# Performance work log

Hardware: AMD Instinct MI355X
Metric: run time of the kernel (lower is better)

## Reference

```python
import jax, jax.numpy as jnp
import numpy as np

# Static configuration (mirrors init_kwargs / forward defaults)
KERNEL = 128          # WW
INDEX_BACK = 32768    # number of highest-frequency bins discarded
PADDING = 0           # padding_count (padding=None in forward)

def next_power2(x):
    return int(2 ** np.ceil(np.log2(x)))

def setup_inputs() -> dict:
    key = jax.random.key(0)
    k1, k2, k3 = jax.random.split(key, 3)
    N, C, W = 32, 8, 65536
    F = 16
    x = jax.random.normal(k1, (N, C, W), dtype=jnp.float32)
    weight = jax.random.normal(k2, (F, C, KERNEL), dtype=jnp.float32) * 0.1
    bias = jax.random.normal(k3, (F,), dtype=jnp.float32)
    return {"x": x, "weight": weight, "bias": bias}

def reference(x, weight, bias):
    # x: [N, C, W], weight: [F, C, WW], bias: [F]
    N, C, W = x.shape
    F, _, WW = weight.shape
    pad = PADDING
    out_W = W - WW + 1 + 2 * pad
    # fft size sized to also hold the backward dout correlation, then next pow2
    init_fft_size_input = W + 2 * pad + 2 * (WW - 1)
    init_fft_size_dout = out_W + 2 * (WW - 1)
    init_fft_size = next_power2(max(init_fft_size_input, init_fft_size_dout))
    half = init_fft_size // 2 + 1

    # rfft with implicit zero-padding to init_fft_size (input left-padded by `pad`)
    x_p = jnp.pad(x, ((0, 0), (0, 0), (pad, 0)))
    xfft = jnp.fft.rfft(x_p, n=init_fft_size, axis=-1)      # [N, C, half]
    yfft = jnp.fft.rfft(weight, n=init_fft_size, axis=-1)   # [F, C, half]

    # spectral compression: drop the INDEX_BACK highest-frequency bins
    keep = half - INDEX_BACK
    xfft = xfft[..., :keep]
    yfft = yfft[..., :keep]

    # cross-correlation in frequency domain (torch conv == correlation),
    # summing over input channels C in the spectrum (linearity of irfft)
    outfft = jnp.einsum('nck,fck->nfk', xfft, jnp.conj(yfft))  # [N, F, keep]

    # zero-pad discarded high frequencies back and invert
    outfft = jnp.pad(outfft, ((0, 0), (0, 0), (0, half - keep)))
    out = jnp.fft.irfft(outfft, n=init_fft_size, axis=-1)[..., :out_W]  # [N, F, out_W]

    out = out + bias[None, :, None]
    return out
```

## Files before the change

kernel.cpp:

```cpp
#include <hip/hip_runtime.h>

namespace {

constexpr int NFFT  = 65536;
constexpr int OUTW  = 65409;
constexpr size_t Y2BYTES = (size_t)256 * 129 * 128 * 8;

typedef float2 cplx;

__device__ __forceinline__ cplx cmk(float x, float y){ return make_float2(x, y); }
__device__ __forceinline__ cplx cadd(cplx a, cplx b){ return cmk(a.x+b.x, a.y+b.y); }
__device__ __forceinline__ cplx csub(cplx a, cplx b){ return cmk(a.x-b.x, a.y-b.y); }
__device__ __forceinline__ cplx cmul(cplx a, cplx b){ return cmk(a.x*b.x - a.y*b.y, a.x*b.y + a.y*b.x); }
__device__ __forceinline__ cplx cmulj(cplx a, cplx b){
  return cmk(a.x*b.x + a.y*b.y, a.y*b.x - a.x*b.y); }

template<int DIR>
__device__ __forceinline__ void dft16(cplx v[16]) {
  const float C1 = 0.92387953251128674f;
  const float S1 = 0.38268343236508977f;
  const float C2 = 0.70710678118654752f;
  const float WR[16]  = {1.f, C1, C2, S1, 0.f, -S1, -C2, -C1, -1.f, -C1, -C2, -S1, 0.f, S1, C2, C1};
  const float WIF[16] = {0.f, -S1, -C2, -C1, -1.f, -C1, -C2, -S1, 0.f, S1, C2, C1, 1.f, C1, C2, S1};
  cplx s[16];
  #pragma unroll
  for (int n2 = 0; n2 < 4; ++n2) {
    cplx a = v[n2], b = v[n2+4], c = v[n2+8], d = v[n2+12];
    cplx ac = cadd(a,c), am = csub(a,c), bd = cadd(b,d), bm = csub(b,d);
    cplx x0 = cadd(ac, bd), x2 = csub(ac, bd), x1, x3;
    if (DIR == -1) { x1 = cmk(am.x + bm.y, am.y - bm.x); x3 = cmk(am.x - bm.y, am.y + bm.x); }
    else           { x1 = cmk(am.x - bm.y, am.y + bm.x); x3 = cmk(am.x + bm.y, am.y - bm.x); }
    s[0*4+n2] = x0;
    {
      int e1 = (n2*1) & 15, e2 = (n2*2) & 15, e3 = (n2*3) & 15;
      cplx w1 = cmk(WR[e1], (DIR==-1)? WIF[e1] : -WIF[e1]);
      cplx w2 = cmk(WR[e2], (DIR==-1)? WIF[e2] : -WIF[e2]);
      cplx w3 = cmk(WR[e3], (DIR==-1)? WIF[e3] : -WIF[e3]);
      s[1*4+n2] = cmul(x1, w1);
      s[2*4+n2] = cmul(x2, w2);
      s[3*4+n2] = cmul(x3, w3);
    }
  }
  #pragma unroll
  for (int t1 = 0; t1 < 4; ++t1) {
    cplx a = s[t1*4+0], b = s[t1*4+1], c = s[t1*4+2], d = s[t1*4+3];
    cplx ac = cadd(a,c), am = csub(a,c), bd = cadd(b,d), bm = csub(b,d);
    cplx x0 = cadd(ac,bd), x2 = csub(ac,bd), x1, x3;
    if (DIR == -1) { x1 = cmk(am.x + bm.y, am.y - bm.x); x3 = cmk(am.x - bm.y, am.y + bm.x); }
    else           { x1 = cmk(am.x - bm.y, am.y + bm.x); x3 = cmk(am.x + bm.y, am.y - bm.x); }
    v[t1+0] = x0; v[t1+4] = x1; v[t1+8] = x2; v[t1+12] = x3;
  }
}

template<int DIR>
__global__ __launch_bounds__(256)
void fft_pass_a(const cplx* __restrict__ in, long inStride, int inLen,
                cplx* __restrict__ T) {
  int blk = blockIdx.x;
  int seq = blk >> 4;
  int B0  = (blk & 15) << 4;
  int t = threadIdx.x;
  __shared__ cplx sm[4608];
  cplx (*tile)[260] = (cplx(*)[260])sm;
  cplx* tile2 = sm;
  {
    const cplx* src = in + (long)seq * inStride;
    int cb = t & 15, rg = t >> 4;
    #pragma unroll
    for (int i = 0; i < 16; ++i) {
      int a = i*16 + rg;
      int sIdx = a*256 + B0 + cb;
      cplx v = (sIdx < inLen) ? src[sIdx] : cmk(0.f, 0.f);
      tile[cb][a] = v;
    }
  }
  __syncthreads();
  int cc = t >> 4, j = t & 15;
  cplx x[16];
  #pragma unroll
  for (int a1 = 0; a1 < 16; ++a1) x[a1] = tile[cc][a1*16 + j];
  dft16<DIR>(x);
  {
    float sn, cs;
    __sincosf((float)DIR * 6.28318530717958648f * (float)j * (1.0f/256.0f), &sn, &cs);
    cplx r = cmk(cs, sn), cur = r;
    #pragma unroll
    for (int t1 = 1; t1 < 16; ++t1) { x[t1] = cmul(x[t1], cur); cur = cmul(cur, r); }
  }
  __syncthreads();
  #pragma unroll
  for (int t1 = 0; t1 < 16; ++t1) tile[cc][t1*16 + ((j + t1) & 15)] = x[t1];
  __syncthreads();
  #pragma unroll
  for (int a2 = 0; a2 < 16; ++a2) x[a2] = tile[cc][j*16 + ((a2 + j) & 15)];
  dft16<DIR>(x);
  int b = B0 + cc;
  __syncthreads();
  {
    float sn, cs;
    __sincosf((float)DIR * 6.28318530717958648f * (float)(b*j) * (1.0f/65536.0f), &sn, &cs);
    cplx cur = cmk(cs, sn);
    __sincosf((float)DIR * 6.28318530717958648f * (float)b * (1.0f/4096.0f), &sn, &cs);
    cplx stp = cmk(cs, sn);
    #pragma unroll
    for (int t2 = 0; t2 < 16; ++t2) {
      tile2[(j + 16*t2)*18 + cc] = cmul(x[t2], cur);
      cur = cmul(cur, stp);
    }
  }
  __syncthreads();
  {
    int rg = t >> 4, cb = t & 15;
    cplx* dst = T + (long)seq * NFFT + B0 + cb;
    #pragma unroll
    for (int i = 0; i < 16; ++i) {
      int k1 = i*16 + rg;
      dst[(long)k1 * 256] = tile2[k1*18 + cb];
    }
  }
}

template<int DIR, int MODE>
__global__ __launch_bounds__(256)
void fft_pass_b(const cplx* __restrict__ T, cplx* __restrict__ outZ,
                float* __restrict__ outR, const float* __restrict__ bias,
                int seqBase) {
  int blk = blockIdx.x;
  int seq = blk >> 4;
  int K0  = (blk & 15) << 4;
  int t = threadIdx.x;
  __shared__ cplx tile[16][260];
  {
    const cplx* src = T + (long)seq * NFFT;
    int ck = t & 15, rg = t >> 4;
    #pragma unroll
    for (int i = 0; i < 16; ++i) {
      int b = i*16 + rg;
      tile[ck][b] = src[b*256 + K0 + ck];
    }
  }
  __syncthreads();
  int cc = t >> 4, j = t & 15;
  cplx x[16];
  #pragma unroll
  for (int a1 = 0; a1 < 16; ++a1) x[a1] = tile[cc][a1*16 + j];
  dft16<DIR>(x);
  {
    float sn, cs;
    __sincosf((float)DIR * 6.28318530717958648f * (float)j * (1.0f/256.0f), &sn, &cs);
    cplx r = cmk(cs, sn), cur = r;
    #pragma unroll
    for (int t1 = 1; t1 < 16; ++t1) { x[t1] = cmul(x[t1], cur); cur = cmul(cur, r); }
  }
  __syncthreads();
  #pragma unroll
  for (int t1 = 0; t1 < 16; ++t1) tile[cc][t1*16 + ((j + t1) & 15)] = x[t1];
  __syncthreads();
  #pragma unroll
  for (int a2 = 0; a2 < 16; ++a2) x[a2] = tile[cc][j*16 + ((a2 + j) & 15)];
  dft16<DIR>(x);
  __syncthreads();
  #pragma unroll
  for (int t2 = 0; t2 < 16; ++t2) tile[cc][j + 16*t2] = x[t2];
  __syncthreads();
  int ck2 = t & 15, rg2 = t >> 4;
  if (MODE == 0) {
    cplx* dst = outZ + (long)seq * NFFT + K0 + ck2;
    #pragma unroll
    for (int i = 0; i < 16; ++i) {
      int k2 = i*16 + rg2;
      dst[256*k2] = tile[ck2][k2];
    }
  } else {
    const float sc = 1.0f / 65536.0f;
    int gseq = seqBase + seq;
    float bf = bias[gseq & 15];
    float* dst = outR + (long)gseq * OUTW;
    #pragma unroll
    for (int i = 0; i < 16; ++i) {
      int k2 = i*16 + rg2;
      int s  = K0 + ck2 + 256*k2;
      int tp = 2*s;
      cplx v = tile[ck2][k2];
      if (tp < OUTW)     dst[tp]   = v.x * sc + bf;
      if (tp + 1 < OUTW) dst[tp+1] = v.y * sc + bf;
    }
  }
}

__global__ __launch_bounds__(256)
void weight_spec(const float* __restrict__ wgt, cplx* __restrict__ Y2) {
  const int k1 = blockIdx.x;
  const int fg = blockIdx.y;
  const int t  = threadIdx.x;
  __shared__ float wt[16][129];
  for (int e = t; e < 16*128; e += 256)
    wt[e >> 7][e & 127] = wgt[(fg*16 + (e >> 7))*128 + (e & 127)];
  __syncthreads();
  const int fcL = t & 15;
  const int fc  = fg*16 + fcL;
  for (int m = t >> 4; m < 129; m += 16) {
    int k = k1 + 256*m;
    if (k > 32768) break;
    float sn, cs;
    __sincosf(-3.14159265358979324f * (float)k * (1.0f/65536.0f), &sn, &cs);
    cplx r  = cmk(cs, sn);
    cplx r2 = cmul(r, r);
    cplx r4 = cmul(r2, r2);
    cplx r8 = cmul(r4, r4);
    cplx av[8];
    #pragma unroll
    for (int v = 0; v < 8; ++v) av[v] = cmk(0.f, 0.f);
    cplx C = cmk(1.f, 0.f);
    #pragma unroll
    for (int u = 0; u < 16; ++u) {
      #pragma unroll
      for (int v = 0; v < 8; ++v) {
        float w = wt[fcL][u*8 + v];
        av[v].x += w * C.x;
        av[v].y += w * C.y;
      }
      C = cmul(C, r8);
    }
    cplx acc = av[7];
    #pragma unroll
    for (int v = 6; v >= 0; --v) acc = cadd(av[v], cmul(r, acc));
    Y2[((long)k1*129 + m)*128 + fc] = acc;
  }
}

__global__ __launch_bounds__(256)
void fused_mid(const cplx* __restrict__ T1, const cplx* __restrict__ Y2,
               cplx* __restrict__ T2) {
  const int ln  = blockIdx.x;
  const int p   = blockIdx.y;
  const int cLo = p;
  const int cHi = (256 - p) & 255;
  const bool selfp = (p == 0) || (p == 128);
  const int t = threadIdx.x;
  const int g = t >> 4;
  const int j = t & 15;
  const int c = g & 7;
  const int half = g >> 3;
  const int col = half ? cHi : cLo;

  __shared__ cplx Ts[16][260];
  __shared__ cplx Xs[8][2][130];

  const float C16 = 0.98078528040323044913f;
  const float S16 = 0.19509032201612826785f;

  cplx x[16];
  {
    const cplx* src = T1 + ((long)(ln*8 + c) * NFFT + (long)col * 256);
    #pragma unroll
    for (int a1 = 0; a1 < 16; ++a1) x[a1] = src[a1*16 + j];
  }
  dft16<-1>(x);
  {
    float sn, cs;
    __sincosf(-6.28318530717958648f * (float)j * (1.0f/256.0f), &sn, &cs);
    cplx r = cmk(cs, sn), cur = r;
    #pragma unroll
    for (int t1 = 1; t1 < 16; ++t1) { x[t1] = cmul(x[t1], cur); cur = cmul(cur, r); }
  }
  #pragma unroll
  for (int t1 = 0; t1 < 16; ++t1) Ts[g][t1*16 + ((j + t1) & 15)] = x[t1];
  #pragma unroll
  for (int a2 = 0; a2 < 16; ++a2) x[a2] = Ts[g][j*16 + ((a2 + j) & 15)];
  dft16<-1>(x);
  #pragma unroll
  for (int t2 = 0; t2 < 16; ++t2) Ts[g][j + 16*t2] = x[t2];
  __syncthreads();

  {
    float sn, cs;
    __sincosf(-3.14159265358979324f * (float)(col + 256*j) * (1.0f/65536.0f), &sn, &cs);
    cplx w = cmk(cs, sn);
    const cplx stp = cmk(C16, -S16);
    #pragma unroll
    for (int t2 = 0; t2 < 8; ++t2) {
      int m = j + 16*t2;
      int k = col + 256*m;
      cplx zk = x[t2];
      int mi = (65536 - k) & 65535;
      cplx zm = Ts[g ^ 8][mi >> 8];
      cplx E = cmk(0.5f*(zk.x + zm.x), 0.5f*(zk.y - zm.y));
      cplx D = cmk(zk.x - zm.x, zk.y + zm.y);
      cplx O = cmk(0.5f*D.y, -0.5f*D.x);
      Xs[c][half][m] = cadd(E, cmul(w, O));
      w = cmul(w, stp);
    }
  }
  if (p == 0 && half == 0 && j == 0) {
    cplx zk = x[8];
    cplx X = cmk(zk.x, -zk.y);
    Xs[c][0][128] = X;
    Xs[c][1][128] = X;
  }
  __syncthreads();

  const int f = g;
  cplx zA[16], zB[16];

#define MAC_PASS(Q, XSEL, ZD, ZM, SRCLANE)                                     \
  do {                                                                         \
    const int q_ = (Q);                                                        \
    float sn_, cs_;                                                            \
    __sincosf(3.14159265358979324f * (float)(q_ + 256*j) * (1.0f/65536.0f),    \
              &sn_, &cs_);                                                     \
    cplx wp = cmk(cs_, sn_);                                                   \
    const cplx stp = cmk(C16, S16);                                            \
    const float4* yb = reinterpret_cast<const float4*>(                        \
        Y2 + ((long)q_*129 + j)*128 + f*8);                                    \
    float4 b0 = yb[0], b1 = yb[1], b2 = yb[2], b3 = yb[3];                     \
    _Pragma("unroll")                                                          \
    for (int t2 = 0; t2 < 8; ++t2) {                                           \
      float4 y0 = b0, y1 = b1, y2 = b2, y3 = b3;                               \
      if (t2 < 7) {                                                            \
        const float4* nx = yb + (long)(t2+1)*1024;                             \
        b0 = nx[0]; b1 = nx[1]; b2 = nx[2]; b3 = nx[3];                        \
      }                                                                        \
      int m = j + 16*t2;                                                       \
      cplx S = cmulj(Xs[0][XSEL][m], cmk(y0.x, y0.y));                         \
      S = cadd(S, cmulj(Xs[1][XSEL][m], cmk(y0.z, y0.w)));                     \
      S = cadd(S, cmulj(Xs[2][XSEL][m], cmk(y1.x, y1.y)));                     \
      S = cadd(S, cmulj(Xs[3][XSEL][m], cmk(y1.z, y1.w)));                     \
      S = cadd(S, cmulj(Xs[4][XSEL][m], cmk(y2.x, y2.y)));                     \
      S = cadd(S, cmulj(Xs[5][XSEL][m], cmk(y2.z, y2.w)));                     \
      S = cadd(S, cmulj(Xs[6][XSEL][m], cmk(y3.x, y3.y)));                     \
      S = cadd(S, cmulj(Xs[7][XSEL][m], cmk(y3.z, y3.w)));                     \
      cplx E2 = cmk(0.5f*S.x, 0.5f*S.y);                                       \
      cplx O2 = cmul(wp, E2);                                                  \
      ZD[t2] = cmk(E2.x - O2.y, E2.y + O2.x);                                  \
      float mx = E2.x + O2.y;                                                  \
      float my = O2.x - E2.y;                                                  \
      mx = __shfl(mx, (SRCLANE));                                              \
      my = __shfl(my, (SRCLANE));                                              \
      ZM[15 - t2] = cmk(mx, my);                                               \
      wp = cmul(wp, stp);                                                      \
    }                                                                          \
  } while (0)

  if (p == 0) {
    int src0 = (t & ~15) | ((16 - j) & 15);
    MAC_PASS(0, 0, zA, zA, src0);
    if (j == 0) {
      zA[15] = zA[14]; zA[14] = zA[13]; zA[13] = zA[12]; zA[12] = zA[11];
      zA[11] = zA[10]; zA[10] = zA[9];  zA[9]  = zA[8];
      const float4* yv = reinterpret_cast<const float4*>(Y2 + (long)128*128 + f*8);
      float4 y0 = yv[0], y1 = yv[1], y2 = yv[2], y3 = yv[3];
      cplx S = cmulj(Xs[0][1][128], cmk(y0.x, y0.y));
      S = cadd(S, cmulj(Xs[1][1][128], cmk(y0.z, y0.w)));
      S = cadd(S, cmulj(Xs[2][1][128], cmk(y1.x, y1.y)));
      S = cadd(S, cmulj(Xs[3][1][128], cmk(y1.z, y1.w)));
      S = cadd(S, cmulj(Xs[4][1][128], cmk(y2.x, y2.y)));
      S = cadd(S, cmulj(Xs[5][1][128], cmk(y2.z, y2.w)));
      S = cadd(S, cmulj(Xs[6][1][128], cmk(y3.x, y3.y)));
      S = cadd(S, cmulj(Xs[7][1][128], cmk(y3.z, y3.w)));
      zA[8] = cmk(S.x, -S.y);
    }
  } else if (selfp) {
    MAC_PASS(128, 0, zA, zA, t ^ 15);
  } else {
    MAC_PASS(cLo, 0, zA, zB, t ^ 15);
    MAC_PASS(cHi, 1, zB, zA, t ^ 15);
  }
#undef MAC_PASS

#define INV_STORE(Z, MCOL)                                                     \
  do {                                                                         \
    dft16<1>(Z);                                                               \
    {                                                                          \
      float sn_, cs_;                                                          \
      __sincosf(6.28318530717958648f * (float)j * (1.0f/256.0f), &sn_, &cs_);  \
      cplx rr = cmk(cs_, sn_), cur = rr;                                       \
      _Pragma("unroll")                                                        \
      for (int t1 = 1; t1 < 16; ++t1) { Z[t1] = cmul(Z[t1], cur); cur = cmul(cur, rr); } \
    }                                                                          \
    _Pragma("unroll")                                                          \
    for (int t1 = 0; t1 < 16; ++t1) Ts[g][t1*16 + ((j + t1) & 15)] = Z[t1];    \
    _Pragma("unroll")                                                          \
    for (int a2 = 0; a2 < 16; ++a2) Z[a2] = Ts[g][j*16 + ((a2 + j) & 15)];     \
    dft16<1>(Z);                                                               \
    {                                                                          \
      float sn_, cs_;                                                          \
      __sincosf(6.28318530717958648f * (float)((MCOL)*j) * (1.0f/65536.0f), &sn_, &cs_); \
      cplx cur = cmk(cs_, sn_);                                                \
      __sincosf(6.28318530717958648f * (float)(MCOL) * (1.0f/4096.0f), &sn_, &cs_); \
      cplx stp2 = cmk(cs_, sn_);                                               \
      cplx* dst = T2 + (long)(ln*16 + f) * NFFT + (long)(MCOL) * 256;          \
      _Pragma("unroll")                                                        \
      for (int t2 = 0; t2 < 16; ++t2) {                                        \
        dst[j + 16*t2] = cmul(Z[t2], cur);                                     \
        cur = cmul(cur, stp2);                                                 \
      }                                                                        \
    }                                                                          \
  } while (0)

  INV_STORE(zA, cLo);
  if (!selfp) INV_STORE(zB, cHi);
#undef INV_STORE
}

}

extern "C" void kernel_launch(void* const* d_in, const int* in_sizes, int n_in,
                              void* d_out, int out_size, void* d_ws, size_t ws_size,
                              hipStream_t stream) {
  const cplx*  x    = (const cplx*)d_in[0];
  const float* wgt  = (const float*)d_in[1];
  const float* bias = (const float*)d_in[2];
  float* out = (float*)d_out;

  static const int BnOpt[5] = {16, 8, 4, 2, 1};
  int Bn = 1;
  for (int i = 0; i < 5; ++i) {
    size_t need = Y2BYTES + (size_t)BnOpt[i] * 12582912ull;
    if (need <= ws_size) { Bn = BnOpt[i]; break; }
  }
  char* ws = (char*)d_ws;
  cplx* Y2 = (cplx*)ws;
  cplx* T1 = (cplx*)(ws + Y2BYTES);
  cplx* T2 = (cplx*)(ws + Y2BYTES + (size_t)Bn * 4194304ull);

  weight_spec<<<dim3(256, 8), dim3(256), 0, stream>>>(wgt, Y2);

  for (int n0 = 0; n0 < 32; n0 += Bn) {
    fft_pass_a<-1><<<dim3(Bn*8*16), dim3(256), 0, stream>>>(
        x + (long)n0*8*32768, 32768, 32768, T1);
    fused_mid<<<dim3(Bn, 129), dim3(256), 0, stream>>>(T1, Y2, T2);
    fft_pass_b<1,1><<<dim3(Bn*16*16), dim3(256), 0, stream>>>(
        T2, (cplx*)nullptr, out, bias, n0*16);
  }
}
```

Measured before the change: 639.3 us.

## Alias fused_mid shared buffers, raise occupancy, remap blocks across XCDs

The Ts and Xs shared arrays in fused_mid now share one buffer. The mirrored values are read into registers first, with extra barriers so the buffer can be reused safely, which cuts LDS use per block. Launch bounds ask for 4 blocks per CU. When Bn is 16, the grid is remapped to 8x258 so that blocks handling the same frequency columns p land on the same XCD, which should improve L2 reuse of Y2. The cost is more register pressure from the zmr array, added barriers, and index arithmetic.

```diff
diff --git a/kernel.cpp b/kernel.cpp
--- a/kernel.cpp
+++ b/kernel.cpp
@@ -229,11 +229,19 @@
   }
 }
 
-__global__ __launch_bounds__(256)
+__global__ __launch_bounds__(256, 4)
 void fused_mid(const cplx* __restrict__ T1, const cplx* __restrict__ Y2,
-               cplx* __restrict__ T2) {
-  const int ln  = blockIdx.x;
-  const int p   = blockIdx.y;
+               cplx* __restrict__ T2, int remap) {
+  int p, ln;
+  if (remap) {
+    int xcd = blockIdx.x;
+    int y   = blockIdx.y;
+    if (y < 256) { p = xcd + 8*(y >> 4); ln = y & 15; }
+    else         { p = 128;            ln = ((y - 256) << 3) | xcd; }
+  } else {
+    ln = blockIdx.x;
+    p  = blockIdx.y;
+  }
   const int cLo = p;
   const int cHi = (256 - p) & 255;
   const bool selfp = (p == 0) || (p == 128);
@@ -244,8 +252,9 @@
   const int half = g >> 3;
   const int col = half ? cHi : cLo;
 
-  __shared__ cplx Ts[16][260];
-  __shared__ cplx Xs[8][2][130];
+  __shared__ cplx sm[16*260];
+  cplx (*Ts)[260]      = (cplx(*)[260])sm;
+  cplx (*Xv)[2][130]   = (cplx(*)[2][130])sm;
 
   const float C16 = 0.98078528040323044913f;
   const float S16 = 0.19509032201612826785f;
@@ -273,6 +282,15 @@
   for (int t2 = 0; t2 < 16; ++t2) Ts[g][j + 16*t2] = x[t2];
   __syncthreads();
 
+  cplx zmr[8];
+  #pragma unroll
+  for (int t2 = 0; t2 < 8; ++t2) {
+    int m = j + 16*t2;
+    int k = col + 256*m;
+    int mi = (65536 - k) & 65535;
+    zmr[t2] = Ts[g ^ 8][mi >> 8];
+  }
+  __syncthreads();
   {
     float sn, cs;
     __sincosf(-3.14159265358979324f * (float)(col + 256*j) * (1.0f/65536.0f), &sn, &cs);
@@ -281,22 +299,20 @@
     #pragma unroll
     for (int t2 = 0; t2 < 8; ++t2) {
       int m = j + 16*t2;
-      int k = col + 256*m;
       cplx zk = x[t2];
-      int mi = (65536 - k) & 65535;
-      cplx zm = Ts[g ^ 8][mi >> 8];
+      cplx zm = zmr[t2];
       cplx E = cmk(0.5f*(zk.x + zm.x), 0.5f*(zk.y - zm.y));
       cplx D = cmk(zk.x - zm.x, zk.y + zm.y);
       cplx O = cmk(0.5f*D.y, -0.5f*D.x);
-      Xs[c][half][m] = cadd(E, cmul(w, O));
+      Xv[c][half][m] = cadd(E, cmul(w, O));
       w = cmul(w, stp);
     }
   }
   if (p == 0 && half == 0 && j == 0) {
     cplx zk = x[8];
     cplx X = cmk(zk.x, -zk.y);
-    Xs[c][0][128] = X;
-    Xs[c][1][128] = X;
+    Xv[c][0][128] = X;
+    Xv[c][1][128] = X;
   }
   __syncthreads();
 
@@ -322,14 +338,14 @@
         b0 = nx[0]; b1 = nx[1]; b2 = nx[2]; b3 = nx[3];                        \
       }                                                                        \
       int m = j + 16*t2;                                                       \
-      cplx S = cmulj(Xs[0][XSEL][m], cmk(y0.x, y0.y));                         \
-      S = cadd(S, cmulj(Xs[1][XSEL][m], cmk(y0.z, y0.w)));                     \
-      S = cadd(S, cmulj(Xs[2][XSEL][m], cmk(y1.x, y1.y)));                     \
-      S = cadd(S, cmulj(Xs[3][XSEL][m], cmk(y1.z, y1.w)));                     \
-      S = cadd(S, cmulj(Xs[4][XSEL][m], cmk(y2.x, y2.y)));                     \
-      S = cadd(S, cmulj(Xs[5][XSEL][m], cmk(y2.z, y2.w)));                     \
-      S = cadd(S, cmulj(Xs[6][XSEL][m], cmk(y3.x, y3.y)));                     \
-      S = cadd(S, cmulj(Xs[7][XSEL][m], cmk(y3.z, y3.w)));                     \
+      cplx S = cmulj(Xv[0][XSEL][m], cmk(y0.x, y0.y));                         \
+      S = cadd(S, cmulj(Xv[1][XSEL][m], cmk(y0.z, y0.w)));                     \
+      S = cadd(S, cmulj(Xv[2][XSEL][m], cmk(y1.x, y1.y)));                     \
+      S = cadd(S, cmulj(Xv[3][XSEL][m], cmk(y1.z, y1.w)));                     \
+      S = cadd(S, cmulj(Xv[4][XSEL][m], cmk(y2.x, y2.y)));                     \
+      S = cadd(S, cmulj(Xv[5][XSEL][m], cmk(y2.z, y2.w)));                     \
+      S = cadd(S, cmulj(Xv[6][XSEL][m], cmk(y3.x, y3.y)));                     \
+      S = cadd(S, cmulj(Xv[7][XSEL][m], cmk(y3.z, y3.w)));                     \
       cplx E2 = cmk(0.5f*S.x, 0.5f*S.y);                                       \
       cplx O2 = cmul(wp, E2);                                                  \
       ZD[t2] = cmk(E2.x - O2.y, E2.y + O2.x);                                  \
@@ -350,14 +366,14 @@
       zA[11] = zA[10]; zA[10] = zA[9];  zA[9]  = zA[8];
       const float4* yv = reinterpret_cast<const float4*>(Y2 + (long)128*128 + f*8);
       float4 y0 = yv[0], y1 = yv[1], y2 = yv[2], y3 = yv[3];
-      cplx S = cmulj(Xs[0][1][128], cmk(y0.x, y0.y));
-      S = cadd(S, cmulj(Xs[1][1][128], cmk(y0.z, y0.w)));
-      S = cadd(S, cmulj(Xs[2][1][128], cmk(y1.x, y1.y)));
-      S = cadd(S, cmulj(Xs[3][1][128], cmk(y1.z, y1.w)));
-      S = cadd(S, cmulj(Xs[4][1][128], cmk(y2.x, y2.y)));
-      S = cadd(S, cmulj(Xs[5][1][128], cmk(y2.z, y2.w)));
-      S = cadd(S, cmulj(Xs[6][1][128], cmk(y3.x, y3.y)));
-      S = cadd(S, cmulj(Xs[7][1][128], cmk(y3.z, y3.w)));
+      cplx S = cmulj(Xv[0][1][128], cmk(y0.x, y0.y));
+      S = cadd(S, cmulj(Xv[1][1][128], cmk(y0.z, y0.w)));
+      S = cadd(S, cmulj(Xv[2][1][128], cmk(y1.x, y1.y)));
+      S = cadd(S, cmulj(Xv[3][1][128], cmk(y1.z, y1.w)));
+      S = cadd(S, cmulj(Xv[4][1][128], cmk(y2.x, y2.y)));
+      S = cadd(S, cmulj(Xv[5][1][128], cmk(y2.z, y2.w)));
+      S = cadd(S, cmulj(Xv[6][1][128], cmk(y3.x, y3.y)));
+      S = cadd(S, cmulj(Xv[7][1][128], cmk(y3.z, y3.w)));
       zA[8] = cmk(S.x, -S.y);
     }
   } else if (selfp) {
@@ -367,6 +383,8 @@
     MAC_PASS(cHi, 1, zB, zA, t ^ 15);
   }
 #undef MAC_PASS
+
+  __syncthreads();
 
 #define INV_STORE(Z, MCOL)                                                     \
   do {                                                                         \
@@ -429,7 +447,10 @@
   for (int n0 = 0; n0 < 32; n0 += Bn) {
     fft_pass_a<-1><<<dim3(Bn*8*16), dim3(256), 0, stream>>>(
         x + (long)n0*8*32768, 32768, 32768, T1);
-    fused_mid<<<dim3(Bn, 129), dim3(256), 0, stream>>>(T1, Y2, T2);
+    if (Bn == 16)
+      fused_mid<<<dim3(8, 258), dim3(256), 0, stream>>>(T1, Y2, T2, 1);
+    else
+      fused_mid<<<dim3(Bn, 129), dim3(256), 0, stream>>>(T1, Y2, T2, 0);
     fft_pass_b<1,1><<<dim3(Bn*16*16), dim3(256), 0, stream>>>(
         T2, (cplx*)nullptr, out, bias, n0*16);
   }
```

Result: slower. 1.121 ms (+75.3%).
